# Performance work log

Measured on AMD Instinct MI355X. Metric: run time of the kernel, lower is better.

## Reference

```python
import jax, jax.numpy as jnp
import numpy as np

N, H, n = 256, 64, 32
EPS = 1e-8  # eigenvalue floor for sqrt/rsqrt/log (SPD by construction, guard fp32)


def _sym_apply(X, fn, clip=True):
    """Apply scalar function fn to the eigenvalues of symmetric X (batched)."""
    w, V = jnp.linalg.eigh(X)
    if clip:
        w = jnp.clip(w, EPS)
    return jnp.einsum('...ij,...j,...kj->...ik', V, fn(w), V)


def _barygeom(Xf):
    """Riemannian barycenter via one Karcher-flow step (m_fun.BaryGeom, k=1).
    Xf: (M, n, n) SPD batch -> (n, n) Frechet mean."""
    G = jnp.mean(Xf, axis=0)                                   # arithmetic init
    G_sq = _sym_apply(G, jnp.sqrt)                             # G^{1/2}
    G_isq = _sym_apply(G, lambda w: 1.0 / jnp.sqrt(w))         # G^{-1/2}
    # mean of log(G^{-1/2} X G^{-1/2}) over the batch
    L = jnp.mean(_sym_apply(G_isq @ Xf @ G_isq, jnp.log), axis=0)
    expL = _sym_apply(L, jnp.exp, clip=False)                  # L symmetric, not PSD
    return G_sq @ expL @ G_sq


def setup_inputs() -> dict:
    key = jax.random.key(0)
    k1, k2 = jax.random.split(key)
    A = jax.random.normal(k1, (N, H, n, n), dtype=jnp.float32)
    # SPD inputs: A A^T / n + 0.1 I  -> well-conditioned covariance-like matrices
    X = jnp.einsum('bhij,bhkj->bhik', A, A) / n \
        + 0.1 * jnp.eye(n, dtype=jnp.float32)
    Bw = jax.random.normal(k2, (n, n), dtype=jnp.float32)
    weight = Bw @ Bw.T / n + 0.1 * jnp.eye(n, dtype=jnp.float32)  # SPD parameter
    return {"X": X, "weight": weight}


def reference(X, weight):
    Nb, Hc, nn_, _ = X.shape
    Xf = X.reshape(Nb * Hc, nn_, nn_)                 # (N*h, n, n), as in forward
    # Frechet mean is computed under torch.no_grad() in the original -> constant
    G = jax.lax.stop_gradient(_barygeom(Xf))
    G_isq = _sym_apply(G, lambda w: 1.0 / jnp.sqrt(w))
    Xc = G_isq @ Xf @ G_isq                           # CongrG(X, mean, 'neg')
    W_sq = _sym_apply(weight, jnp.sqrt)
    out = W_sq @ Xc @ W_sq                            # CongrG(Xc, weight, 'pos')
    return out.reshape(Nb, Hc, nn_, nn_)
```

## Files before the change

### kernel.cpp

```cpp
#include <hip/hip_runtime.h>
#include <math.h>

#define NMAT   16384
#define CHEB_A 0.08
#define CHEB_B 7.0
#define DDEG   29
#define NCOEF  (DDEG + 1)
#define NITER  ((DDEG - 1) / 2)
#define NLOGBLK 2048
#define NWAVES (NLOGBLK * 4)

#define WS_GQ    0
#define WS_GSQ   1024
#define WS_C     2112
#define WS_CT    3136

#define OUT_PA   0
#define OUT_PL   262144
#define OUT_PL2  2359296

typedef __attribute__((ext_vector_type(8)))  short short8;
typedef __attribute__((ext_vector_type(16))) float f32x16;
typedef __attribute__((ext_vector_type(2)))  float f32x2;
typedef __attribute__((ext_vector_type(2)))  __bf16 bf16x2;

union FB { short8 v; unsigned int w[4]; };

#define ROWOF(r, h) (((r) & 3) + 8 * ((r) >> 2) + 4 * (h))

__device__ __forceinline__ unsigned int pk2(float a, float b) {
    unsigned int au = __float_as_uint(a) + 0x8000u;
    unsigned int bu = __float_as_uint(b) + 0x8000u;
    return __builtin_amdgcn_perm(bu, au, 0x07060302u);
}
__device__ __forceinline__ float rhi(float x) {
    return __uint_as_float((__float_as_uint(x) + 0x8000u) & 0xffff0000u);
}

__device__ __forceinline__ unsigned int cvt2(float a, float b) {
    f32x2 s; s.x = a; s.y = b;
    bf16x2 t = __builtin_convertvector(s, bf16x2);
    unsigned int r;
    __builtin_memcpy(&r, &t, 4);
    return r;
}

template <bool HALF>
__device__ __forceinline__ void toB(const f32x16& d, FB& b1, FB& b2) {
    unsigned int p[8];
#pragma unroll
    for (int g = 0; g < 8; ++g) {
        float s0 = HALF ? 0.5f * d[2 * g]     : d[2 * g];
        float s1 = HALF ? 0.5f * d[2 * g + 1] : d[2 * g + 1];
        p[g] = cvt2(s0, s1);
    }
    auto r02 = __builtin_amdgcn_permlane32_swap(p[0], p[2], false, false);
    auto r13 = __builtin_amdgcn_permlane32_swap(p[1], p[3], false, false);
    auto r46 = __builtin_amdgcn_permlane32_swap(p[4], p[6], false, false);
    auto r57 = __builtin_amdgcn_permlane32_swap(p[5], p[7], false, false);
    b1.w[0] = r02[0]; b1.w[1] = r13[0]; b1.w[2] = r02[1]; b1.w[3] = r13[1];
    b2.w[0] = r46[0]; b2.w[1] = r57[0]; b2.w[2] = r46[1]; b2.w[3] = r57[1];
}

#define MFMA(a, b, c) __builtin_amdgcn_mfma_f32_32x32x16_bf16((a), (b), (c), 0, 0, 0)

struct SplitM { FB h1, h2, l1, l2; };

__device__ __forceinline__ void splitB(const f32x16& d, SplitM& s) {
    unsigned int ph[8], pl[8];
#pragma unroll
    for (int g = 0; g < 8; ++g) {
        float a = d[2 * g], b = d[2 * g + 1];
        ph[g] = pk2(a, b);
        pl[g] = pk2(a - rhi(a), b - rhi(b));
    }
    auto h02 = __builtin_amdgcn_permlane32_swap(ph[0], ph[2], false, false);
    auto h13 = __builtin_amdgcn_permlane32_swap(ph[1], ph[3], false, false);
    auto h46 = __builtin_amdgcn_permlane32_swap(ph[4], ph[6], false, false);
    auto h57 = __builtin_amdgcn_permlane32_swap(ph[5], ph[7], false, false);
    s.h1.w[0] = h02[0]; s.h1.w[1] = h13[0]; s.h1.w[2] = h02[1]; s.h1.w[3] = h13[1];
    s.h2.w[0] = h46[0]; s.h2.w[1] = h57[0]; s.h2.w[2] = h46[1]; s.h2.w[3] = h57[1];
    auto l02 = __builtin_amdgcn_permlane32_swap(pl[0], pl[2], false, false);
    auto l13 = __builtin_amdgcn_permlane32_swap(pl[1], pl[3], false, false);
    auto l46 = __builtin_amdgcn_permlane32_swap(pl[4], pl[6], false, false);
    auto l57 = __builtin_amdgcn_permlane32_swap(pl[5], pl[7], false, false);
    s.l1.w[0] = l02[0]; s.l1.w[1] = l13[0]; s.l1.w[2] = l02[1]; s.l1.w[3] = l13[1];
    s.l2.w[0] = l46[0]; s.l2.w[1] = l57[0]; s.l2.w[2] = l46[1]; s.l2.w[3] = l57[1];
}

__device__ __forceinline__ f32x16 mulSS(const SplitM& A, const SplitM& B) {
    f32x16 d;
#pragma unroll
    for (int r = 0; r < 16; ++r) d[r] = 0.f;
    d = MFMA(A.h2.v, B.l2.v, d); d = MFMA(A.h1.v, B.l1.v, d);
    d = MFMA(A.l2.v, B.h2.v, d); d = MFMA(A.l1.v, B.h1.v, d);
    d = MFMA(A.h2.v, B.h2.v, d); d = MFMA(A.h1.v, B.h1.v, d);
    return d;
}

__device__ __forceinline__ float wred(float v) {
    v += __shfl_xor(v, 32);
    v += __shfl_xor(v, 16);
    v += __shfl_xor(v, 8);
    v += __shfl_xor(v, 4);
    v += __shfl_xor(v, 2);
    v += __shfl_xor(v, 1);
    return v;
}

__device__ __forceinline__ void mm32(const float* A, const float* B, float* D, int t) {
    int i = t >> 3, j0 = (t & 7) * 4;
    float a[32];
#pragma unroll
    for (int q = 0; q < 8; ++q) {
        float4 v = *(const float4*)&A[i * 32 + q * 4];
        a[4 * q] = v.x; a[4 * q + 1] = v.y; a[4 * q + 2] = v.z; a[4 * q + 3] = v.w;
    }
    float ax = 0.f, ay = 0.f, az = 0.f, aw = 0.f;
#pragma unroll
    for (int k = 0; k < 32; ++k) {
        float4 bv = *(const float4*)&B[k * 32 + j0];
        ax += a[k] * bv.x; ay += a[k] * bv.y; az += a[k] * bv.z; aw += a[k] * bv.w;
    }
    float4 r = { ax, ay, az, aw };
    *(float4*)&D[i * 32 + j0] = r;
}

__global__ __launch_bounds__(256) void k_psum(const float4* __restrict__ X4,
                                              float4* __restrict__ pA4) {
    int b = blockIdx.x, t = threadIdx.x;
    float4 acc = { 0.f, 0.f, 0.f, 0.f };
    for (int r = 0; r < 64; ++r) {
        float4 v = X4[(size_t)(b * 64 + r) * 256 + t];
        acc.x += v.x; acc.y += v.y; acc.z += v.z; acc.w += v.w;
    }
    pA4[b * 256 + t] = acc;
}

__global__ __launch_bounds__(256) void k_setup(const float4* __restrict__ pA4,
                                               float* __restrict__ ws) {
    __shared__ alignas(16) float sG[1024], sE[1024], sPa[1024], sPb[1024], sS1[1024], sS2[1024];
    __shared__ float sc[2];
    int t = threadIdx.x;
    float4 acc = { 0.f, 0.f, 0.f, 0.f };
    for (int b = 0; b < 256; ++b) {
        float4 v = pA4[b * 256 + t];
        acc.x += v.x; acc.y += v.y; acc.z += v.z; acc.w += v.w;
    }
    const float invM = 1.0f / (float)NMAT;
    sG[4 * t + 0] = acc.x * invM; sG[4 * t + 1] = acc.y * invM;
    sG[4 * t + 2] = acc.z * invM; sG[4 * t + 3] = acc.w * invM;
    __syncthreads();
    if (t == 0) { float s = 0.f; for (int d = 0; d < 32; ++d) s += sG[d * 33]; sc[0] = s / 32.0f; }
    __syncthreads();
    float c = sc[0];
    int i = t >> 3, j0 = (t & 7) * 4;
#pragma unroll
    for (int q = 0; q < 4; ++q) {
        int e = i * 32 + j0 + q;
        sE[e] = sG[e] / c - ((i == j0 + q) ? 1.f : 0.f);
    }
    __syncthreads();
    const float alp[9] = { 1.f, 0.5f, -0.125f, 0.0625f, -0.0390625f, 0.02734375f,
                           -0.0205078125f, 0.01611328125f, -0.013092041015625f };
    const float bet[9] = { 1.f, -0.5f, 0.375f, -0.3125f, 0.2734375f, -0.24609375f,
                           0.2255859375f, -0.20947265625f, 0.196380615234375f };
#pragma unroll
    for (int q = 0; q < 4; ++q) {
        int e = i * 32 + j0 + q;
        float d = (i == j0 + q) ? 1.f : 0.f;
        sS1[e] = d + alp[1] * sE[e];
        sS2[e] = d + bet[1] * sE[e];
        sPa[e] = sE[e];
    }
    __syncthreads();
    {
        float* P = sPa; float* Pn = sPb;
        for (int k = 2; k <= 8; ++k) {
            mm32(P, sE, Pn, t);
            __syncthreads();
#pragma unroll
            for (int q = 0; q < 4; ++q) {
                int e = i * 32 + j0 + q;
                sS1[e] += alp[k] * Pn[e];
                sS2[e] += bet[k] * Pn[e];
            }
            float* tmp = P; P = Pn; Pn = tmp;
            __syncthreads();
        }
    }
    float rc = sqrtf(c);
#pragma unroll
    for (int q = 0; q < 4; ++q) {
        int e = i * 32 + j0 + q;
        ws[WS_GSQ + e] = rc * sS1[e];
        ws[WS_GQ + e]  = sS2[e] / rc;
    }
}

__global__ __launch_bounds__(256, 2) void k_logsum(const float* __restrict__ Xg,
                                                   const float* __restrict__ ws,
                                                   float* __restrict__ pL) {
    __shared__ float sLacc[1024];
    __shared__ float scheb[NCOEF];
    int t = threadIdx.x;
    for (int e = t; e < 1024; e += 256) sLacc[e] = 0.f;
    if (t < NCOEF) {
        float alpha = 0.5f * (float)(CHEB_A + CHEB_B);
        float beta  = 0.5f * (float)(CHEB_B - CHEB_A);
        float dd = beta / alpha, s = sqrtf(1.f - dd * dd), tt = dd / (1.f + s);
        float v;
        if (t == 0) v = 2.f * (logf(alpha) + logf(0.5f * (1.f + s)));
        else        v = 2.f * ((t & 1) ? 1.f : -1.f) * exp2f((float)t * log2f(tt)) / (float)t;
        scheb[t] = v;
    }
    const int wv = t >> 6, lane = t & 63, h = lane >> 5, col = lane & 31;

    int hasd = (((col >> 2) & 1) == h);
    int dreg = 4 * (col >> 3) + (col & 3);
    f32x16 dm;
#pragma unroll
    for (int r = 0; r < 16; ++r) dm[r] = (hasd && r == dreg) ? 1.f : 0.f;

    const float* Gqp = ws + WS_GQ + col * 32 + 8 * h;
    float4 ga = *(const float4*)(Gqp);
    float4 gb = *(const float4*)(Gqp + 4);
    float4 gc = *(const float4*)(Gqp + 16);
    float4 gd = *(const float4*)(Gqp + 20);
    FB GqH1, GqH2, GqL1, GqL2;
    GqH1.w[0] = pk2(ga.x, ga.y); GqH1.w[1] = pk2(ga.z, ga.w);
    GqH1.w[2] = pk2(gb.x, gb.y); GqH1.w[3] = pk2(gb.z, gb.w);
    GqH2.w[0] = pk2(gc.x, gc.y); GqH2.w[1] = pk2(gc.z, gc.w);
    GqH2.w[2] = pk2(gd.x, gd.y); GqH2.w[3] = pk2(gd.z, gd.w);
    GqL1.w[0] = pk2(ga.x - rhi(ga.x), ga.y - rhi(ga.y));
    GqL1.w[1] = pk2(ga.z - rhi(ga.z), ga.w - rhi(ga.w));
    GqL1.w[2] = pk2(gb.x - rhi(gb.x), gb.y - rhi(gb.y));
    GqL1.w[3] = pk2(gb.z - rhi(gb.z), gb.w - rhi(gb.w));
    GqL2.w[0] = pk2(gc.x - rhi(gc.x), gc.y - rhi(gc.y));
    GqL2.w[1] = pk2(gc.z - rhi(gc.z), gc.w - rhi(gc.w));
    GqL2.w[2] = pk2(gd.x - rhi(gd.x), gd.y - rhi(gd.y));
    GqL2.w[3] = pk2(gd.z - rhi(gd.z), gd.w - rhi(gd.w));
    __syncthreads();

    const float m2v = 2.0f / (float)(CHEB_B - CHEB_A);
    const float shv = (float)((CHEB_A + CHEB_B) / (CHEB_B - CHEB_A));
    const float tm = 2.f * m2v, tsh = -2.f * shv;
    const float cDv = scheb[DDEG], c0h = 0.5f * scheb[0];

    FB CDB1, CDB2;
    {
        f32x16 cDdm;
#pragma unroll
        for (int r = 0; r < 16; ++r) cDdm[r] = cDv * dm[r];
        toB<false>(cDdm, CDB1, CDB2);
    }

    const int m0 = blockIdx.x * 4 + wv;
    const int m1 = m0 + NWAVES;

    const float* Xma = Xg + (size_t)m0 * 1024 + col * 32 + 8 * h;
    const float* Xmb = Xg + (size_t)m1 * 1024 + col * 32 + 8 * h;
    float4 a0 = *(const float4*)(Xma);
    float4 a1 = *(const float4*)(Xma + 4);
    float4 a2 = *(const float4*)(Xma + 16);
    float4 a3 = *(const float4*)(Xma + 20);
    float4 b0 = *(const float4*)(Xmb);
    float4 b1v = *(const float4*)(Xmb + 4);
    float4 b2v = *(const float4*)(Xmb + 16);
    float4 b3v = *(const float4*)(Xmb + 20);
    FB AXa1, AXa2, AXb1, AXb2;
    AXa1.w[0] = cvt2(a0.x, a0.y); AXa1.w[1] = cvt2(a0.z, a0.w);
    AXa1.w[2] = cvt2(a1.x, a1.y); AXa1.w[3] = cvt2(a1.z, a1.w);
    AXa2.w[0] = cvt2(a2.x, a2.y); AXa2.w[1] = cvt2(a2.z, a2.w);
    AXa2.w[2] = cvt2(a3.x, a3.y); AXa2.w[3] = cvt2(a3.z, a3.w);
    AXb1.w[0] = cvt2(b0.x, b0.y); AXb1.w[1] = cvt2(b0.z, b0.w);
    AXb1.w[2] = cvt2(b1v.x, b1v.y); AXb1.w[3] = cvt2(b1v.z, b1v.w);
    AXb2.w[0] = cvt2(b2v.x, b2v.y); AXb2.w[1] = cvt2(b2v.z, b2v.w);
    AXb2.w[2] = cvt2(b3v.x, b3v.y); AXb2.w[3] = cvt2(b3v.z, b3v.w);

    f32x16 Ua, Ub;
#pragma unroll
    for (int r = 0; r < 16; ++r) { Ua[r] = 0.f; Ub[r] = 0.f; }
    Ua = MFMA(AXa2.v, GqL2.v, Ua); Ub = MFMA(AXb2.v, GqL2.v, Ub);
    Ua = MFMA(AXa1.v, GqL1.v, Ua); Ub = MFMA(AXb1.v, GqL1.v, Ub);
    Ua = MFMA(AXa2.v, GqH2.v, Ua); Ub = MFMA(AXb2.v, GqH2.v, Ub);
    Ua = MFMA(AXa1.v, GqH1.v, Ua); Ub = MFMA(AXb1.v, GqH1.v, Ub);
    FB Ba1, Ba2, Bb1, Bb2;
    toB<false>(Ua, Ba1, Ba2);
    toB<false>(Ub, Bb1, Bb2);
    f32x16 Sa, Sb;
#pragma unroll
    for (int r = 0; r < 16; ++r) { Sa[r] = 0.f; Sb[r] = 0.f; }
    Sa = MFMA(GqL2.v, Ba2.v, Sa); Sb = MFMA(GqL2.v, Bb2.v, Sb);
    Sa = MFMA(GqL1.v, Ba1.v, Sa); Sb = MFMA(GqL1.v, Bb1.v, Sb);
    Sa = MFMA(GqH2.v, Ba2.v, Sa); Sb = MFMA(GqH2.v, Bb2.v, Sb);
    Sa = MFMA(GqH1.v, Ba1.v, Sa); Sb = MFMA(GqH1.v, Bb1.v, Sb);
    f32x16 Ta, Tb;
#pragma unroll
    for (int r = 0; r < 16; ++r) {
        Ta[r] = fmaf(tm, Sa[r], tsh * dm[r]);
        Tb[r] = fmaf(tm, Sb[r], tsh * dm[r]);
    }
    FB Aa1, Aa2, Ab1, Ab2;
    toB<false>(Ta, Aa1, Aa2);
    toB<false>(Tb, Ab1, Ab2);

    f32x16 X0a, X1a, X0b, X1b;
#pragma unroll
    for (int r = 0; r < 16; ++r) {
        X1a[r] = cDv * dm[r]; X0a[r] = 0.f;
        X1b[r] = cDv * dm[r]; X0b[r] = 0.f;
    }
    Ba1 = CDB1; Ba2 = CDB2; Bb1 = CDB1; Bb2 = CDB2;
    for (int it = 0; it < NITER; ++it) {
        float ka = scheb[DDEG - 1 - 2 * it];
        float kb = scheb[DDEG - 2 - 2 * it];
#pragma unroll
        for (int r = 0; r < 16; ++r) {
            X0a[r] = fmaf(ka, dm[r], -X0a[r]);
            X0b[r] = fmaf(ka, dm[r], -X0b[r]);
        }
        X0a = MFMA(Aa2.v, Ba2.v, X0a); X0b = MFMA(Ab2.v, Bb2.v, X0b);
        X0a = MFMA(Aa1.v, Ba1.v, X0a); X0b = MFMA(Ab1.v, Bb1.v, X0b);
        toB<false>(X0a, Ba1, Ba2);
        toB<false>(X0b, Bb1, Bb2);
#pragma unroll
        for (int r = 0; r < 16; ++r) {
            X1a[r] = fmaf(kb, dm[r], -X1a[r]);
            X1b[r] = fmaf(kb, dm[r], -X1b[r]);
        }
        X1a = MFMA(Aa2.v, Ba2.v, X1a); X1b = MFMA(Ab2.v, Bb2.v, X1b);
        X1a = MFMA(Aa1.v, Ba1.v, X1a); X1b = MFMA(Ab1.v, Bb1.v, X1b);
        if (it < NITER - 1) {
            toB<false>(X1a, Ba1, Ba2);
            toB<false>(X1b, Bb1, Bb2);
        } else {
            toB<true>(X1a, Ba1, Ba2);
            toB<true>(X1b, Bb1, Bb2);
        }
    }
#pragma unroll
    for (int r = 0; r < 16; ++r) {
        X0a[r] = fmaf(c0h, dm[r], -X0a[r]);
        X0b[r] = fmaf(c0h, dm[r], -X0b[r]);
    }
    X0a = MFMA(Aa2.v, Ba2.v, X0a); X0b = MFMA(Ab2.v, Bb2.v, X0b);
    X0a = MFMA(Aa1.v, Ba1.v, X0a); X0b = MFMA(Ab1.v, Bb1.v, X0b);

    f32x16 Facc;
#pragma unroll
    for (int r = 0; r < 16; ++r) Facc[r] = X0a[r] + X0b[r];

#pragma unroll
    for (int r = 0; r < 16; ++r) {
        int row = (r & 3) + 8 * (r >> 2) + 4 * h;
        atomicAdd(&sLacc[row * 32 + col], Facc[r]);
    }
    __syncthreads();
    float4 v = *(float4*)&sLacc[4 * t];
    ((float4*)pL)[(size_t)blockIdx.x * 256 + t] = v;
}

__global__ __launch_bounds__(256) void k_red32(const float4* __restrict__ pL4,
                                               float4* __restrict__ pL24) {
    int b = blockIdx.x, t = threadIdx.x;
    float4 acc = { 0.f, 0.f, 0.f, 0.f };
    for (int r = 0; r < 64; ++r) {
        float4 v = pL4[(size_t)(b * 64 + r) * 256 + t];
        acc.x += v.x; acc.y += v.y; acc.z += v.z; acc.w += v.w;
    }
    pL24[b * 256 + t] = acc;
}

__global__ __launch_bounds__(256) void k_final(const float4* __restrict__ pL24,
                                               const float* __restrict__ Wg,
                                               float* __restrict__ ws) {
    __shared__ alignas(16) float sL[1024];
    int t = threadIdx.x;
    {
        float4 acc = { 0.f, 0.f, 0.f, 0.f };
        for (int b = 0; b < 32; ++b) {
            float4 v = pL24[b * 256 + t];
            acc.x += v.x; acc.y += v.y; acc.z += v.z; acc.w += v.w;
        }
        const float invM = 1.0f / (float)NMAT;
        sL[4 * t + 0] = acc.x * invM; sL[4 * t + 1] = acc.y * invM;
        sL[4 * t + 2] = acc.z * invM; sL[4 * t + 3] = acc.w * invM;
    }
    __syncthreads();
    if (t >= 64) return;

    const int h = t >> 5, col = t & 31;
    const int hasd = (((col >> 2) & 1) == h);
    const int dreg = 4 * (col >> 3) + (col & 3);
    f32x16 dm;
#pragma unroll
    for (int r = 0; r < 16; ++r) dm[r] = (hasd && r == dreg) ? 1.f : 0.f;

    f32x16 Lm;
#pragma unroll
    for (int r = 0; r < 16; ++r) Lm[r] = sL[ROWOF(r, h) * 32 + col];

    float tr = 0.f;
#pragma unroll
    for (int r = 0; r < 16; ++r) tr = fmaf(Lm[r], dm[r], tr);
    float s0 = wred(tr) / 32.0f;

    f32x16 L0;
#pragma unroll
    for (int r = 0; r < 16; ++r) L0[r] = fmaf(-s0, dm[r], Lm[r]);

    SplitM SL0; splitB(L0, SL0);
    f32x16 E4;
#pragma unroll
    for (int r = 0; r < 16; ++r) E4[r] = dm[r] + L0[r];
    SplitM SP = SL0;
    for (int k = 2; k <= 12; ++k) {
        f32x16 Pn = mulSS(SP, SL0);
        float invk = 1.0f / (float)k;
#pragma unroll
        for (int r = 0; r < 16; ++r) { Pn[r] *= invk; E4[r] += Pn[r]; }
        if (k < 12) splitB(Pn, SP);
    }
    float es = expf(s0);
#pragma unroll
    for (int r = 0; r < 16; ++r) E4[r] *= es;

    f32x16 Gs;
#pragma unroll
    for (int r = 0; r < 16; ++r) Gs[r] = ws[WS_GSQ + ROWOF(r, h) * 32 + col];
    SplitM SG; splitB(Gs, SG);
    SplitM SE; splitB(E4, SE);
    f32x16 Mx = mulSS(SE, SG);
    SplitM SM; splitB(Mx, SM);
    f32x16 Gn = mulSS(SG, SM);

    float tr2 = 0.f;
#pragma unroll
    for (int r = 0; r < 16; ++r) tr2 = fmaf(Gn[r], dm[r], tr2);
    float c2 = wred(tr2) / 32.0f;
    float ic2 = 1.0f / c2;

    f32x16 YC, ZC;
#pragma unroll
    for (int r = 0; r < 16; ++r) { YC[r] = Gn[r] * ic2; ZC[r] = dm[r]; }
    SplitM SY, SZ, ST;
    splitB(YC, SY); splitB(ZC, SZ);
    for (int it = 0; it < 8; ++it) {
        f32x16 ZY = mulSS(SZ, SY);
        f32x16 T;
#pragma unroll
        for (int r = 0; r < 16; ++r) T[r] = fmaf(1.5f, dm[r], -0.5f * ZY[r]);
        splitB(T, ST);
        f32x16 Yn = mulSS(SY, ST);
        f32x16 Zn = mulSS(ST, SZ);
        YC = Yn; ZC = Zn;
        splitB(YC, SY); splitB(ZC, SZ);
    }
    float rc2 = rsqrtf(c2);
    f32x16 Gi;
#pragma unroll
    for (int r = 0; r < 16; ++r) Gi[r] = ZC[r] * rc2;
    SplitM SGi; splitB(Gi, SGi);

    f32x16 Wm;
#pragma unroll
    for (int r = 0; r < 16; ++r) Wm[r] = Wg[ROWOF(r, h) * 32 + col];
    float ss = 0.f;
#pragma unroll
    for (int r = 0; r < 16; ++r) ss = fmaf(Wm[r], Wm[r], ss);
    float c3 = sqrtf(wred(ss));
    float ic3 = 1.0f / c3;
#pragma unroll
    for (int r = 0; r < 16; ++r) { YC[r] = Wm[r] * ic3; ZC[r] = dm[r]; }
    splitB(YC, SY); splitB(ZC, SZ);
    for (int it = 0; it < 15; ++it) {
        f32x16 ZY = mulSS(SZ, SY);
        f32x16 T;
#pragma unroll
        for (int r = 0; r < 16; ++r) T[r] = fmaf(1.5f, dm[r], -0.5f * ZY[r]);
        splitB(T, ST);
        f32x16 Yn = mulSS(SY, ST);
        f32x16 Zn = mulSS(ST, SZ);
        YC = Yn; ZC = Zn;
        splitB(YC, SY); splitB(ZC, SZ);
    }
    float rc3 = sqrtf(c3);
    f32x16 Ws;
#pragma unroll
    for (int r = 0; r < 16; ++r) Ws[r] = YC[r] * rc3;
    SplitM SW; splitB(Ws, SW);

    f32x16 C = mulSS(SW, SGi);
#pragma unroll
    for (int r = 0; r < 16; ++r) {
        int row = ROWOF(r, h);
        ws[WS_C + row * 32 + col] = C[r];
        ws[WS_CT + col * 32 + row] = C[r];
    }
}

__global__ __launch_bounds__(256) void k_out(const float* __restrict__ Xg,
                                             const float* __restrict__ ws,
                                             float* __restrict__ Og) {
    __shared__ alignas(16) float sCT[1024];
    __shared__ alignas(16) float sX[1024];
    __shared__ alignas(16) float sTt[33 * 32];
    int t = threadIdx.x;
    int i = t >> 3, j0 = (t & 7) * 4;
    for (int e = t; e < 1024; e += 256) sCT[e] = ws[WS_CT + e];
    __syncthreads();
    for (int r = 0; r < 8; ++r) {
        int m = blockIdx.x * 8 + r;
        const float4* Xm4 = (const float4*)(Xg + (size_t)m * 1024);
        *(float4*)&sX[4 * t] = Xm4[t];
        __syncthreads();
        float ax = 0.f, ay = 0.f, az = 0.f, aw = 0.f;
#pragma unroll
        for (int k = 0; k < 32; ++k) {
            float cv = sCT[k * 32 + i];
            float4 xv = *(const float4*)&sX[k * 32 + j0];
            ax += cv * xv.x; ay += cv * xv.y; az += cv * xv.z; aw += cv * xv.w;
        }
        sTt[(j0 + 0) * 33 + i] = ax; sTt[(j0 + 1) * 33 + i] = ay;
        sTt[(j0 + 2) * 33 + i] = az; sTt[(j0 + 3) * 33 + i] = aw;
        __syncthreads();
        ax = ay = az = aw = 0.f;
#pragma unroll
        for (int k = 0; k < 32; ++k) {
            float tv = sTt[k * 33 + i];
            float4 cv = *(const float4*)&sCT[k * 32 + j0];
            ax += tv * cv.x; ay += tv * cv.y; az += tv * cv.z; aw += tv * cv.w;
        }
        float4 r4 = { ax, ay, az, aw };
        *(float4*)&Og[(size_t)m * 1024 + i * 32 + j0] = r4;
        __syncthreads();
    }
}

extern "C" void kernel_launch(void* const* d_in, const int* in_sizes, int n_in,
                              void* d_out, int out_size, void* d_ws, size_t ws_size,
                              hipStream_t stream) {
    const float* X = (const float*)d_in[0];
    const float* W = (const float*)d_in[1];
    float* out = (float*)d_out;
    float* ws  = (float*)d_ws;
    float* pA  = out + OUT_PA;
    float* pL  = out + OUT_PL;
    float* pL2 = out + OUT_PL2;

    hipLaunchKernelGGL(k_psum,   dim3(256),     dim3(256), 0, stream, (const float4*)X, (float4*)pA);
    hipLaunchKernelGGL(k_setup,  dim3(1),       dim3(256), 0, stream, (const float4*)pA, ws);
    hipLaunchKernelGGL(k_logsum, dim3(NLOGBLK), dim3(256), 0, stream, X, ws, pL);
    hipLaunchKernelGGL(k_red32,  dim3(32),      dim3(256), 0, stream, (const float4*)pL, (float4*)pL2);
    hipLaunchKernelGGL(k_final,  dim3(1),       dim3(256), 0, stream, (const float4*)pL2, W, ws);
    hipLaunchKernelGGL(k_out,    dim3(2048),    dim3(256), 0, stream, X, ws, out);
}
```

Measured before the change: 280.6 us.

## Rewrite output congruence with split-bf16 MFMA and raise logsum occupancy

The final C·X·Cᵀ congruence kernel drops its LDS-staged scalar FP32 matmuls. Each wave now loads X directly into registers as hi/lo bf16 splits and does two split-precision MFMA products, using a grid-stride loop over 1024 blocks. k_logsum's launch bounds go from 2 to 3 blocks per CU, and the precomputed constant B operand is dropped and rebuilt in place to save registers. The risks are some precision loss from the 3-term bf16 split, uncoalesced scalar output stores, and register spills at the higher occupancy target.

```diff
diff --git a/kernel.cpp b/kernel.cpp
--- a/kernel.cpp
+++ b/kernel.cpp
@@ -9,6 +9,8 @@
 #define NITER  ((DDEG - 1) / 2)
 #define NLOGBLK 2048
 #define NWAVES (NLOGBLK * 4)
+#define NOUTBLK 1024
+#define NOUTWV  (NOUTBLK * 4)
 
 #define WS_GQ    0
 #define WS_GSQ   1024
@@ -98,6 +100,27 @@
     return d;
 }
 
+__device__ __forceinline__ void loadSplit(const float* __restrict__ base,
+                                          int col, int h, SplitM& s) {
+    const float* p = base + col * 32 + 8 * h;
+    float4 a = *(const float4*)(p);
+    float4 b = *(const float4*)(p + 4);
+    float4 c = *(const float4*)(p + 16);
+    float4 d = *(const float4*)(p + 20);
+    s.h1.w[0] = pk2(a.x, a.y); s.h1.w[1] = pk2(a.z, a.w);
+    s.h1.w[2] = pk2(b.x, b.y); s.h1.w[3] = pk2(b.z, b.w);
+    s.h2.w[0] = pk2(c.x, c.y); s.h2.w[1] = pk2(c.z, c.w);
+    s.h2.w[2] = pk2(d.x, d.y); s.h2.w[3] = pk2(d.z, d.w);
+    s.l1.w[0] = pk2(a.x - rhi(a.x), a.y - rhi(a.y));
+    s.l1.w[1] = pk2(a.z - rhi(a.z), a.w - rhi(a.w));
+    s.l1.w[2] = pk2(b.x - rhi(b.x), b.y - rhi(b.y));
+    s.l1.w[3] = pk2(b.z - rhi(b.z), b.w - rhi(b.w));
+    s.l2.w[0] = pk2(c.x - rhi(c.x), c.y - rhi(c.y));
+    s.l2.w[1] = pk2(c.z - rhi(c.z), c.w - rhi(c.w));
+    s.l2.w[2] = pk2(d.x - rhi(d.x), d.y - rhi(d.y));
+    s.l2.w[3] = pk2(d.z - rhi(d.z), d.w - rhi(d.w));
+}
+
 __device__ __forceinline__ float wred(float v) {
     v += __shfl_xor(v, 32);
     v += __shfl_xor(v, 16);
@@ -198,7 +221,7 @@
     }
 }
 
-__global__ __launch_bounds__(256, 2) void k_logsum(const float* __restrict__ Xg,
+__global__ __launch_bounds__(256, 3) void k_logsum(const float* __restrict__ Xg,
                                                    const float* __restrict__ ws,
                                                    float* __restrict__ pL) {
     __shared__ float sLacc[1024];
@@ -222,38 +245,18 @@
 #pragma unroll
     for (int r = 0; r < 16; ++r) dm[r] = (hasd && r == dreg) ? 1.f : 0.f;
 
-    const float* Gqp = ws + WS_GQ + col * 32 + 8 * h;
-    float4 ga = *(const float4*)(Gqp);
-    float4 gb = *(const float4*)(Gqp + 4);
-    float4 gc = *(const float4*)(Gqp + 16);
-    float4 gd = *(const float4*)(Gqp + 20);
     FB GqH1, GqH2, GqL1, GqL2;
-    GqH1.w[0] = pk2(ga.x, ga.y); GqH1.w[1] = pk2(ga.z, ga.w);
-    GqH1.w[2] = pk2(gb.x, gb.y); GqH1.w[3] = pk2(gb.z, gb.w);
-    GqH2.w[0] = pk2(gc.x, gc.y); GqH2.w[1] = pk2(gc.z, gc.w);
-    GqH2.w[2] = pk2(gd.x, gd.y); GqH2.w[3] = pk2(gd.z, gd.w);
-    GqL1.w[0] = pk2(ga.x - rhi(ga.x), ga.y - rhi(ga.y));
-    GqL1.w[1] = pk2(ga.z - rhi(ga.z), ga.w - rhi(ga.w));
-    GqL1.w[2] = pk2(gb.x - rhi(gb.x), gb.y - rhi(gb.y));
-    GqL1.w[3] = pk2(gb.z - rhi(gb.z), gb.w - rhi(gb.w));
-    GqL2.w[0] = pk2(gc.x - rhi(gc.x), gc.y - rhi(gc.y));
-    GqL2.w[1] = pk2(gc.z - rhi(gc.z), gc.w - rhi(gc.w));
-    GqL2.w[2] = pk2(gd.x - rhi(gd.x), gd.y - rhi(gd.y));
-    GqL2.w[3] = pk2(gd.z - rhi(gd.z), gd.w - rhi(gd.w));
+    {
+        SplitM SGq;
+        loadSplit(ws + WS_GQ, col, h, SGq);
+        GqH1 = SGq.h1; GqH2 = SGq.h2; GqL1 = SGq.l1; GqL2 = SGq.l2;
+    }
     __syncthreads();
 
     const float m2v = 2.0f / (float)(CHEB_B - CHEB_A);
     const float shv = (float)((CHEB_A + CHEB_B) / (CHEB_B - CHEB_A));
     const float tm = 2.f * m2v, tsh = -2.f * shv;
     const float cDv = scheb[DDEG], c0h = 0.5f * scheb[0];
-
-    FB CDB1, CDB2;
-    {
-        f32x16 cDdm;
-#pragma unroll
-        for (int r = 0; r < 16; ++r) cDdm[r] = cDv * dm[r];
-        toB<false>(cDdm, CDB1, CDB2);
-    }
 
     const int m0 = blockIdx.x * 4 + wv;
     const int m1 = m0 + NWAVES;
@@ -311,7 +314,8 @@
         X1a[r] = cDv * dm[r]; X0a[r] = 0.f;
         X1b[r] = cDv * dm[r]; X0b[r] = 0.f;
     }
-    Ba1 = CDB1; Ba2 = CDB2; Bb1 = CDB1; Bb2 = CDB2;
+    toB<false>(X1a, Ba1, Ba2);
+    Bb1 = Ba1; Bb2 = Ba2;
     for (int it = 0; it < NITER; ++it) {
         float ka = scheb[DDEG - 1 - 2 * it];
         float kb = scheb[DDEG - 2 - 2 * it];
@@ -503,38 +507,22 @@
 __global__ __launch_bounds__(256) void k_out(const float* __restrict__ Xg,
                                              const float* __restrict__ ws,
                                              float* __restrict__ Og) {
-    __shared__ alignas(16) float sCT[1024];
-    __shared__ alignas(16) float sX[1024];
-    __shared__ alignas(16) float sTt[33 * 32];
     int t = threadIdx.x;
-    int i = t >> 3, j0 = (t & 7) * 4;
-    for (int e = t; e < 1024; e += 256) sCT[e] = ws[WS_CT + e];
-    __syncthreads();
-    for (int r = 0; r < 8; ++r) {
-        int m = blockIdx.x * 8 + r;
-        const float4* Xm4 = (const float4*)(Xg + (size_t)m * 1024);
-        *(float4*)&sX[4 * t] = Xm4[t];
-        __syncthreads();
-        float ax = 0.f, ay = 0.f, az = 0.f, aw = 0.f;
-#pragma unroll
-        for (int k = 0; k < 32; ++k) {
-            float cv = sCT[k * 32 + i];
-            float4 xv = *(const float4*)&sX[k * 32 + j0];
-            ax += cv * xv.x; ay += cv * xv.y; az += cv * xv.z; aw += cv * xv.w;
+    const int wv = t >> 6, lane = t & 63, h = lane >> 5, col = lane & 31;
+    SplitM SCt;
+    loadSplit(ws + WS_C, col, h, SCt);
+
+    for (int m = blockIdx.x * 4 + wv; m < NMAT; m += NOUTWV) {
+        SplitM SX;
+        loadSplit(Xg + (size_t)m * 1024, col, h, SX);
+        f32x16 V = mulSS(SX, SCt);
+        SplitM SV; splitB(V, SV);
+        f32x16 O = mulSS(SCt, SV);
+        float* Om = Og + (size_t)m * 1024;
+#pragma unroll
+        for (int r = 0; r < 16; ++r) {
+            Om[ROWOF(r, h) * 32 + col] = O[r];
         }
-        sTt[(j0 + 0) * 33 + i] = ax; sTt[(j0 + 1) * 33 + i] = ay;
-        sTt[(j0 + 2) * 33 + i] = az; sTt[(j0 + 3) * 33 + i] = aw;
-        __syncthreads();
-        ax = ay = az = aw = 0.f;
-#pragma unroll
-        for (int k = 0; k < 32; ++k) {
-            float tv = sTt[k * 33 + i];
-            float4 cv = *(const float4*)&sCT[k * 32 + j0];
-            ax += tv * cv.x; ay += tv * cv.y; az += tv * cv.z; aw += tv * cv.w;
-        }
-        float4 r4 = { ax, ay, az, aw };
-        *(float4*)&Og[(size_t)m * 1024 + i * 32 + j0] = r4;
-        __syncthreads();
     }
 }
 
@@ -554,5 +542,5 @@
     hipLaunchKernelGGL(k_logsum, dim3(NLOGBLK), dim3(256), 0, stream, X, ws, pL);
     hipLaunchKernelGGL(k_red32,  dim3(32),      dim3(256), 0, stream, (const float4*)pL, (float4*)pL2);
     hipLaunchKernelGGL(k_final,  dim3(1),       dim3(256), 0, stream, (const float4*)pL2, W, ws);
-    hipLaunchKernelGGL(k_out,    dim3(2048),    dim3(256), 0, stream, X, ws, out);
-}
+    hipLaunchKernelGGL(k_out,    dim3(NOUTBLK), dim3(256), 0, stream, X, ws, out);
+}
```

Result: faster. 250.1 us (-10.8%).
